# Kernel optimization log

Hardware: AMD Instinct MI355X
Metric: run time of the kernel (lower is better)

## Reference

```python
import jax, jax.numpy as jnp
import numpy as np

N, E, B = 50000, 400000, 8
ND, ED, H, L = 32, 16, 128, 3

def setup_inputs() -> dict:
    key = jax.random.key(0)
    ks = jax.random.split(key, 32)
    s = 0.05
    inp = {
        'x': jax.random.normal(ks[0], (N, ND), jnp.float32),
        'edge_attr': jax.random.normal(ks[1], (E, ED), jnp.float32),
        'global_feature': jax.random.normal(ks[2], (B, 1), jnp.float32),
        'edge_index': jax.random.randint(ks[3], (2, E), 0, N, jnp.int64),
        'batch': jnp.sort(jax.random.randint(ks[4], (N,), 0, B, jnp.int64)),
        # embeddings
        'Wn': jax.random.normal(ks[5], (ND, H), jnp.float32) * s,
        'bn': jnp.zeros((H,), jnp.float32),
        'We': jax.random.normal(ks[6], (ED, H), jnp.float32) * s,
        'be': jnp.zeros((H,), jnp.float32),
        'Wg': jax.random.normal(ks[7], (1, H), jnp.float32) * s,
        'bg': jnp.zeros((H,), jnp.float32),
        # message-passing layers (stacked over L)
        'mW1': jax.random.normal(ks[8], (L, 3 * H, H), jnp.float32) * s,
        'mb1': jnp.zeros((L, H), jnp.float32),
        'mW2': jax.random.normal(ks[9], (L, H, H), jnp.float32) * s,
        'mb2': jnp.zeros((L, H), jnp.float32),
        'uW1': jax.random.normal(ks[10], (L, 2 * H, H), jnp.float32) * s,
        'ub1': jnp.zeros((L, H), jnp.float32),
        'uW2': jax.random.normal(ks[11], (L, H, H), jnp.float32) * s,
        'ub2': jnp.zeros((L, H), jnp.float32),
        # readout MLP
        'rW1': jax.random.normal(ks[12], (2 * H, H), jnp.float32) * s,
        'rb1': jnp.zeros((H,), jnp.float32),
        'rW2': jax.random.normal(ks[13], (H, H // 2), jnp.float32) * s,
        'rb2': jnp.zeros((H // 2,), jnp.float32),
        'rW3': jax.random.normal(ks[14], (H // 2, 1), jnp.float32) * s,
        'rb3': jnp.zeros((1,), jnp.float32),
    }
    return inp

def reference(x, edge_attr, global_feature, Wn, bn, We, be, Wg, bg,
              mW1, mb1, mW2, mb2, uW1, ub1, uW2, ub2,
              rW1, rb1, rW2, rb2, rW3, rb3, edge_index, batch):
    h = x @ Wn + bn                      # [N,H]
    e = edge_attr @ We + be              # [E,H]
    g = global_feature @ Wg + bg         # [B,H]
    src, dst = edge_index[0], edge_index[1]  # PyG: x_j=source, x_i=target, aggregate at target
    for l in range(L):
        m_in = jnp.concatenate([h[dst], h[src], e], axis=1)            # [E,3H]
        m = jax.nn.relu(m_in @ mW1[l] + mb1[l]) @ mW2[l] + mb2[l]       # [E,H]
        aggr = jax.ops.segment_sum(m, dst, num_segments=N)              # [N,H]
        u_in = jnp.concatenate([h, aggr], axis=1)                       # [N,2H]
        upd = jax.nn.relu(u_in @ uW1[l] + ub1[l]) @ uW2[l] + ub2[l]
        h = h + upd
    counts = jax.ops.segment_sum(jnp.ones((N,), h.dtype), batch, num_segments=B)
    pooled = jax.ops.segment_sum(h, batch, num_segments=B) / jnp.maximum(counts, 1.0)[:, None]
    final = jnp.concatenate([pooled, g], axis=1)                        # [B,2H]
    out = jax.nn.relu(final @ rW1 + rb1)
    out = jax.nn.relu(out @ rW2 + rb2)
    return out @ rW3 + rb3                                              # [B,1]
```

## Files before the change

### kernel.cpp

```cpp
#include <hip/hip_runtime.h>

#define NN 50000
#define NPAD 50048
#define NBLK 391
#define NE 400000
#define NBATCH 8
#define NDIM 32
#define EDIM 16
#define H 128
#define NLAYERS 3
#define CHUNK_ELEMS 4096
#define NODE_CHUNKS 24
#define ZW_CHUNK 8192
#define NSB 196
#define ZEB 128

typedef __attribute__((ext_vector_type(8))) __bf16 bf16x8;
typedef __attribute__((ext_vector_type(16))) float f32x16;
typedef __attribute__((ext_vector_type(8))) short short8;
typedef __attribute__((ext_vector_type(2))) float v2f;

__device__ __forceinline__ void block_sync_lds() {
  asm volatile("s_waitcnt lgkmcnt(0)\ns_barrier" ::: "memory");
}
__device__ __forceinline__ void wait_lds() {
  asm volatile("s_waitcnt lgkmcnt(0)" ::: "memory");
}
__device__ __forceinline__ v2f bf2f(unsigned u) {
  v2f r;
  r.x = __uint_as_float(u << 16);
  r.y = __uint_as_float(u & 0xffff0000u);
  return r;
}

__global__ __launch_bounds__(128) void embed_nodes_kernel(
    const float* __restrict__ x, const float* __restrict__ Wn,
    const float* __restrict__ bn, __bf16* __restrict__ hb) {
  __shared__ float Ws[NDIM * H];
  __shared__ float xs[16 * NDIM];
  int j = threadIdx.x;
  int nbase = blockIdx.x * 16;
  for (int r = 0; r < NDIM; ++r) Ws[r * H + j] = Wn[r * H + j];
#pragma unroll
  for (int t = 0; t < 4; ++t) {
    int f = j + t * 128;
    xs[f] = x[nbase * NDIM + f];
  }
  __syncthreads();
  float b = bn[j];
  for (int nn = 0; nn < 16; ++nn) {
    float acc = b;
#pragma unroll
    for (int k = 0; k < NDIM; ++k)
      acc = fmaf(xs[nn * NDIM + k], Ws[k * H + j], acc);
    hb[(size_t)(nbase + nn) * H + j] = (__bf16)acc;
  }
}

__global__ __launch_bounds__(256) void degree_kernel(const int* __restrict__ ei,
                                                     int* __restrict__ deg) {
  int e = blockIdx.x * 256 + threadIdx.x;
  if (e < NE) atomicAdd(&deg[ei[NE + e]], 1);
}

__global__ __launch_bounds__(256) void scan1_kernel(const int* __restrict__ deg,
                                                    int* __restrict__ bsum) {
  __shared__ int ws[4];
  int i = blockIdx.x * 256 + threadIdx.x;
  int lane = threadIdx.x & 63, wid = threadIdx.x >> 6;
  int v = (i < NN) ? deg[i] : 0;
#pragma unroll
  for (int off = 32; off; off >>= 1) v += __shfl_down(v, off);
  if (lane == 0) ws[wid] = v;
  __syncthreads();
  if (threadIdx.x == 0) bsum[blockIdx.x] = ws[0] + ws[1] + ws[2] + ws[3];
}

__global__ __launch_bounds__(256) void scan2_kernel(const int* __restrict__ bsum,
                                                    int* __restrict__ boff) {
  __shared__ int s[256];
  int t = threadIdx.x;
  int v = (t < NSB) ? bsum[t] : 0;
  s[t] = v;
  __syncthreads();
  for (int off = 1; off < 256; off <<= 1) {
    int u = (t >= off) ? s[t - off] : 0;
    __syncthreads();
    s[t] += u;
    __syncthreads();
  }
  if (t < NSB) boff[t] = s[t] - v;
}

__global__ __launch_bounds__(256) void scan3_kernel(const int* __restrict__ deg,
                                                    const int* __restrict__ boff,
                                                    int* __restrict__ cursor) {
  __shared__ int wsum[4], woff[4];
  int i = blockIdx.x * 256 + threadIdx.x;
  int lane = threadIdx.x & 63, wid = threadIdx.x >> 6;
  int orig = (i < NN) ? deg[i] : 0;
  int v = orig;
#pragma unroll
  for (int off = 1; off < 64; off <<= 1) {
    int u = __shfl_up(v, off);
    if (lane >= off) v += u;
  }
  if (lane == 63) wsum[wid] = v;
  __syncthreads();
  if (threadIdx.x == 0) {
    int r = 0;
#pragma unroll
    for (int w = 0; w < 4; ++w) {
      woff[w] = r;
      r += wsum[w];
    }
  }
  __syncthreads();
  if (i < NN) cursor[i] = (v - orig) + woff[wid] + boff[blockIdx.x];
}

__global__ __launch_bounds__(256) void scatter_kernel(
    const int* __restrict__ ei, int* __restrict__ cursor,
    int* __restrict__ srcSrt, int* __restrict__ eidSrt) {
  int e = blockIdx.x * 256 + threadIdx.x;
  if (e < NE) {
    int d = ei[NE + e];
    int pos = atomicAdd(&cursor[d], 1);
    srcSrt[pos] = ei[e];
    eidSrt[pos] = e;
  }
}

__global__ __launch_bounds__(256) void gather_ea_kernel(
    const float* __restrict__ ea, const int* __restrict__ eidSrt,
    __bf16* __restrict__ eaSrt) {
  int fl = blockIdx.x * 256 + threadIdx.x;
  if (fl < NE) {
    int e = eidSrt[fl];
    const float4* ep = (const float4*)(ea + (size_t)e * EDIM);
    __bf16* op = eaSrt + (size_t)fl * EDIM;
#pragma unroll
    for (int q = 0; q < 4; ++q) {
      float4 v = ep[q];
      op[q * 4 + 0] = (__bf16)v.x;
      op[q * 4 + 1] = (__bf16)v.y;
      op[q * 4 + 2] = (__bf16)v.z;
      op[q * 4 + 3] = (__bf16)v.w;
    }
  }
}

__global__ __launch_bounds__(256) void precomp_zw_kernel(
    const float* __restrict__ mW1, __bf16* __restrict__ ZW) {
  int l = blockIdx.x / 8;
  int c = blockIdx.x % 8;
  int tid = threadIdx.x;
  const float* w1 = mW1 + (size_t)l * 384 * H;
  __bf16* dst = ZW + ((size_t)l * 8 + c) * ZW_CHUNK;
  for (int it = 0; it < 32; ++it) {
    int flat = it * 256 + tid;
    int j = flat & 7;
    int lane = (flat >> 3) & 63;
    int nt = (flat >> 9) & 7;
    int hilo = flat >> 12;
    int k = c * 16 + ((lane >> 5) << 3) + j;
    int n = nt * 32 + (lane & 31);
    float w = (n < 128) ? w1[(size_t)k * H + n]
                        : w1[(size_t)(128 + k) * H + (n - 128)];
    __bf16 hi = (__bf16)w;
    __bf16 lo = (__bf16)(w - (float)hi);
    dst[flat] = hilo ? lo : hi;
  }
}

__global__ __launch_bounds__(128) void precomp_wef_kernel(
    const float* __restrict__ mW1, const float* __restrict__ mb1,
    const float* __restrict__ We, const float* __restrict__ be,
    float* __restrict__ Wef, float* __restrict__ bm) {
  int l = blockIdx.x;
  int n = threadIdx.x;
  const float* w1 = mW1 + (size_t)l * 384 * H;
  float acc[EDIM];
#pragma unroll
  for (int i = 0; i < EDIM; ++i) acc[i] = 0.f;
  float accb = 0.f;
  for (int c = 0; c < H; ++c) {
    float wv = w1[(size_t)(256 + c) * H + n];
    accb = fmaf(be[c], wv, accb);
#pragma unroll
    for (int i = 0; i < EDIM; ++i)
      acc[i] = fmaf(We[i * H + c], wv, acc[i]);
  }
#pragma unroll
  for (int i = 0; i < EDIM; ++i)
    Wef[((size_t)l * EDIM + i) * H + n] = acc[i];
  bm[l * H + n] = mb1[l * H + n] + accb;
}

__global__ __launch_bounds__(256) void precomp_wefs_kernel(
    const float* __restrict__ Wef, __bf16* __restrict__ WefS) {
  int l = blockIdx.x;
  int tid = threadIdx.x;
  int nt = tid >> 6, lane = tid & 63;
  int n = nt * 32 + (lane & 31);
  int half = lane >> 5;
  const float* wl = Wef + (size_t)l * EDIM * H;
  __bf16* dst = WefS + (size_t)l * CHUNK_ELEMS;
#pragma unroll
  for (int j = 0; j < 8; ++j) {
    int k = half * 8 + j;
    float w = wl[(size_t)k * H + n];
    __bf16 hi = (__bf16)w;
    __bf16 lo = (__bf16)(w - (float)hi);
    dst[((0 * 4 + nt) * 64 + lane) * 8 + j] = hi;
    dst[((1 * 4 + nt) * 64 + lane) * 8 + j] = lo;
  }
}

__global__ __launch_bounds__(128) void precomp_wu_kernel(
    const float* __restrict__ uW1, const float* __restrict__ mW2,
    const float* __restrict__ mb2, float* __restrict__ Wu,
    float* __restrict__ va) {
  int l = blockIdx.x / 257;
  int r = blockIdx.x % 257;
  int j = threadIdx.x;
  const float* u1 = uW1 + (size_t)l * 256 * H;
  if (r < 128) {
    Wu[((size_t)l * 256 + r) * H + j] = u1[(size_t)r * H + j];
  } else if (r < 256) {
    int i = r - 128;
    const float* m2 = mW2 + ((size_t)l * H + i) * H;
    float s = 0.f;
    for (int c = 0; c < H; ++c)
      s = fmaf(m2[c], u1[(size_t)(128 + c) * H + j], s);
    Wu[((size_t)l * 256 + r) * H + j] = s;
  } else {
    float s = 0.f;
    for (int c = 0; c < H; ++c)
      s = fmaf(mb2[l * H + c], u1[(size_t)(128 + c) * H + j], s);
    va[l * H + j] = s;
  }
}

__global__ __launch_bounds__(256) void precomp_wns_kernel(
    const float* __restrict__ Wu, const float* __restrict__ uW2,
    __bf16* __restrict__ WnS) {
  int l = blockIdx.x / NODE_CHUNKS;
  int c = blockIdx.x % NODE_CHUNKS;
  int tid = threadIdx.x;
  int nt = tid >> 6, lane = tid & 63;
  int n = nt * 32 + (lane & 31);
  int half = lane >> 5;
  __bf16* dst = WnS + ((size_t)l * NODE_CHUNKS + c) * CHUNK_ELEMS;
#pragma unroll
  for (int j = 0; j < 8; ++j) {
    float w;
    if (c < 16) {
      int k = c * 16 + half * 8 + j;
      w = Wu[((size_t)l * 256 + k) * H + n];
    } else {
      int k = (c - 16) * 16 + half * 8 + j;
      w = uW2[((size_t)l * H + k) * H + n];
    }
    __bf16 hi = (__bf16)w;
    __bf16 lo = (__bf16)(w - (float)hi);
    dst[((0 * 4 + nt) * 64 + lane) * 8 + j] = hi;
    dst[((1 * 4 + nt) * 64 + lane) * 8 + j] = lo;
  }
}

__global__ __launch_bounds__(256) void zdzs_kernel(
    const __bf16* __restrict__ hb, const __bf16* __restrict__ ZW,
    const float* __restrict__ bm, __bf16* __restrict__ z) {
  __shared__ __align__(16) __bf16 Bt[2][ZW_CHUNK];
  int tid = threadIdx.x;
  int wid = tid >> 6, lane = tid & 63, m = lane & 31, half = lane >> 5;
  int nb = blockIdx.x * 128;
  int row = nb + wid * 32 + m;
  const __bf16* aH = hb + (size_t)row * H + half * 8;
  const short8* gW = (const short8*)ZW;
  short8* sB0 = (short8*)&Bt[0][0];
  short8* sB1 = (short8*)&Bt[1][0];
#pragma unroll
  for (int q = 0; q < 4; ++q) sB0[tid + q * 256] = gW[tid + q * 256];
  short8 p0 = gW[1024 + tid], p1 = gW[1024 + tid + 256];
  short8 p2 = gW[1024 + tid + 512], p3 = gW[1024 + tid + 768];
  f32x16 acc[8];
#pragma unroll
  for (int nt = 0; nt < 8; ++nt)
#pragma unroll
    for (int r = 0; r < 16; ++r) acc[nt][r] = 0.f;
  bf16x8 a = *(const bf16x8*)aH;
  block_sync_lds();

  for (int s = 0; s < 8; ++s) {
    int buf = s & 1;
    bf16x8 na = a;
    if (s + 1 < 8) na = *(const bf16x8*)(aH + (s + 1) * 16);
    if (s + 1 < 8) {
      short8* sb = buf ? sB0 : sB1;
      sb[tid] = p0;
      sb[tid + 256] = p1;
      sb[tid + 512] = p2;
      sb[tid + 768] = p3;
      if (s + 2 < 8) {
        p0 = gW[(size_t)(s + 2) * 1024 + tid];
        p1 = gW[(size_t)(s + 2) * 1024 + tid + 256];
        p2 = gW[(size_t)(s + 2) * 1024 + tid + 512];
        p3 = gW[(size_t)(s + 2) * 1024 + tid + 768];
      }
    }
    const __bf16* bb = &Bt[buf][0];
#pragma unroll
    for (int nt = 0; nt < 8; ++nt) {
      bf16x8 bh = *(const bf16x8*)&bb[((0 * 8 + nt) * 64 + lane) * 8];
      bf16x8 bl = *(const bf16x8*)&bb[((1 * 8 + nt) * 64 + lane) * 8];
      acc[nt] = __builtin_amdgcn_mfma_f32_32x32x16_bf16(a, bh, acc[nt], 0, 0, 0);
      acc[nt] = __builtin_amdgcn_mfma_f32_32x32x16_bf16(a, bl, acc[nt], 0, 0, 0);
    }
    a = na;
    if (s + 1 < 8) block_sync_lds();
  }

  float bmv[4];
#pragma unroll
  for (int nt = 0; nt < 4; ++nt) bmv[nt] = bm[nt * 32 + m];
#pragma unroll
  for (int nt = 0; nt < 8; ++nt) {
    float bias = (nt < 4) ? bmv[nt] : 0.f;
#pragma unroll
    for (int r = 0; r < 16; ++r) {
      int rowi = (r & 3) + 8 * (r >> 2) + 4 * half;
      z[(size_t)(nb + wid * 32 + rowi) * 256 + nt * 32 + m] =
          (__bf16)(acc[nt][r] + bias);
    }
  }
}

__global__ __launch_bounds__(256) void ze_kernel(
    const __bf16* __restrict__ eaSrt, const __bf16* __restrict__ WefS,
    __bf16* __restrict__ zePre) {
  __shared__ __align__(16) __bf16 Bf[CHUNK_ELEMS];
  int tid = threadIdx.x;
  ((short8*)Bf)[tid] = ((const short8*)WefS)[tid];
  ((short8*)Bf)[tid + 256] = ((const short8*)WefS)[tid + 256];
  int wid = tid >> 6, lane = tid & 63, m = lane & 31, half = lane >> 5;
  int ebase = blockIdx.x * ZEB + wid * 32;
  bf16x8 a = *(const bf16x8*)(eaSrt + (size_t)(ebase + m) * EDIM + half * 8);
  f32x16 acc[4];
#pragma unroll
  for (int nt = 0; nt < 4; ++nt)
#pragma unroll
    for (int r = 0; r < 16; ++r) acc[nt][r] = 0.f;
  block_sync_lds();
#pragma unroll
  for (int nt = 0; nt < 4; ++nt) {
    bf16x8 bh = *(const bf16x8*)&Bf[((0 * 4 + nt) * 64 + lane) * 8];
    bf16x8 bl = *(const bf16x8*)&Bf[((1 * 4 + nt) * 64 + lane) * 8];
    acc[nt] = __builtin_amdgcn_mfma_f32_32x32x16_bf16(a, bh, acc[nt], 0, 0, 0);
    acc[nt] = __builtin_amdgcn_mfma_f32_32x32x16_bf16(a, bl, acc[nt], 0, 0, 0);
  }
#pragma unroll
  for (int nt = 0; nt < 4; ++nt) {
#pragma unroll
    for (int r = 0; r < 16; ++r) {
      int rowi = (r & 3) + 8 * (r >> 2) + 4 * half;
      zePre[(size_t)(ebase + rowi) * H + nt * 32 + m] = (__bf16)acc[nt][r];
    }
  }
}

__global__ __launch_bounds__(256) void edge_aggr_kernel(
    const __bf16* __restrict__ z, const int* __restrict__ srcSrt,
    const int* __restrict__ cend, const __bf16* __restrict__ zePre,
    float* __restrict__ aggrH) {
  int node = blockIdx.x * 4 + (threadIdx.x >> 6);
  int lane = threadIdx.x & 63;
  int c0 = lane * 2;
  int end = cend[node];
  int start = node ? cend[node - 1] : 0;
  v2f acc = {0.f, 0.f};
  if (start < end) {
    v2f zd = bf2f(*(const unsigned*)(z + (size_t)node * 256 + c0));
    int sArr[4];
#pragma unroll
    for (int p = 0; p < 4; ++p)
      if (start + p < end) sArr[p] = srcSrt[start + p];
    for (int e0 = start; e0 < end; e0 += 4) {
      unsigned zsb[4], zeb[4];
#pragma unroll
      for (int p = 0; p < 4; ++p) {
        if (e0 + p < end) {
          zsb[p] = *(const unsigned*)(z + (size_t)sArr[p] * 256 + 128 + c0);
          zeb[p] = *(const unsigned*)(zePre + (size_t)(e0 + p) * H + c0);
        }
      }
#pragma unroll
      for (int p = 0; p < 4; ++p)
        if (e0 + 4 + p < end) sArr[p] = srcSrt[e0 + 4 + p];
#pragma unroll
      for (int p = 0; p < 4; ++p) {
        if (e0 + p < end) {
          v2f t = zd + bf2f(zsb[p]) + bf2f(zeb[p]);
          acc.x += fmaxf(t.x, 0.f);
          acc.y += fmaxf(t.y, 0.f);
        }
      }
    }
  }
  *(v2f*)(aggrH + (size_t)node * H + c0) = acc;
}

__global__ __launch_bounds__(256) void node_update_mfma_kernel(
    __bf16* __restrict__ hb, const float* __restrict__ aggrH,
    const int* __restrict__ deg, const __bf16* __restrict__ WnS,
    const float* __restrict__ ub1, const float* __restrict__ va,
    const float* __restrict__ ub2) {
  __shared__ __align__(16) __bf16 Bt[2][CHUNK_ELEMS];
  __shared__ __bf16 hid[2][32][132];
  __shared__ float degS[64];
  int tid = threadIdx.x;
  int nb = blockIdx.x * 64;
  if (tid < 64) degS[tid] = (float)deg[nb + tid];
  int wid = tid >> 6, lane = tid & 63, m = lane & 31, half = lane >> 5;
  int rg = wid & 1;
  int nh = wid >> 1;
  int row = nb + rg * 32 + m;
  const __bf16* aHb = hb + (size_t)row * H + half * 8;
  const float* aG = aggrH + (size_t)row * H + half * 8;
  const short8* gW = (const short8*)WnS;
  short8* sB0 = (short8*)&Bt[0][0];
  short8* sB1 = (short8*)&Bt[1][0];
  sB0[tid] = gW[tid];
  sB0[tid + 256] = gW[tid + 256];
  short8 p0 = gW[512 + tid], p1 = gW[512 + tid + 256];
  float bv1[2], bva[2];
#pragma unroll
  for (int ntl = 0; ntl < 2; ++ntl) {
    int nt = nh * 2 + ntl;
    bv1[ntl] = ub1[nt * 32 + m];
    bva[ntl] = va[nt * 32 + m];
  }
  f32x16 acc[2];
#pragma unroll
  for (int ntl = 0; ntl < 2; ++ntl)
#pragma unroll
    for (int r = 0; r < 16; ++r) acc[ntl][r] = 0.f;
  bf16x8 acur = *(const bf16x8*)aHb;
  block_sync_lds();

  for (int s = 0; s < 16; ++s) {
    int buf = s & 1;
    bf16x8 anext = acur;
    if (s + 1 < 16) {
      int sp = s + 1;
      if (sp < 8) {
        anext = *(const bf16x8*)(aHb + sp * 16);
      } else {
        const float* pp = aG + (sp - 8) * 16;
        float4 f0 = *(const float4*)pp;
        float4 f1 = *(const float4*)(pp + 4);
        float af[8] = {f0.x, f0.y, f0.z, f0.w, f1.x, f1.y, f1.z, f1.w};
#pragma unroll
        for (int j = 0; j < 8; ++j) anext[j] = (__bf16)af[j];
      }
    }
    {
      short8* sb = buf ? sB0 : sB1;
      sb[tid] = p0;
      sb[tid + 256] = p1;
      if (s + 2 < NODE_CHUNKS) {
        p0 = gW[(size_t)(s + 2) * 512 + tid];
        p1 = gW[(size_t)(s + 2) * 512 + tid + 256];
      }
    }
    const __bf16* bb = &Bt[buf][0];
#pragma unroll
    for (int ntl = 0; ntl < 2; ++ntl) {
      int nt = nh * 2 + ntl;
      bf16x8 bh = *(const bf16x8*)&bb[((0 * 4 + nt) * 64 + lane) * 8];
      bf16x8 bl = *(const bf16x8*)&bb[((1 * 4 + nt) * 64 + lane) * 8];
      acc[ntl] = __builtin_amdgcn_mfma_f32_32x32x16_bf16(acur, bh, acc[ntl], 0, 0, 0);
      acc[ntl] = __builtin_amdgcn_mfma_f32_32x32x16_bf16(acur, bl, acc[ntl], 0, 0, 0);
    }
    acur = anext;
    block_sync_lds();
  }

#pragma unroll
  for (int ntl = 0; ntl < 2; ++ntl) {
    int nt = nh * 2 + ntl;
#pragma unroll
    for (int r = 0; r < 16; ++r) {
      int rowi = (r & 3) + 8 * (r >> 2) + 4 * half;
      float v = acc[ntl][r] + bv1[ntl] + degS[rg * 32 + rowi] * bva[ntl];
      hid[rg][rowi][nt * 32 + m] = (__bf16)fmaxf(v, 0.f);
      acc[ntl][r] = 0.f;
    }
  }
  block_sync_lds();

  for (int s = 16; s < NODE_CHUNKS; ++s) {
    int buf = s & 1;
    if (s + 1 < NODE_CHUNKS) {
      short8* sb = buf ? sB0 : sB1;
      sb[tid] = p0;
      sb[tid + 256] = p1;
      if (s + 2 < NODE_CHUNKS) {
        p0 = gW[(size_t)(s + 2) * 512 + tid];
        p1 = gW[(size_t)(s + 2) * 512 + tid + 256];
      }
    }
    bf16x8 ah = *(const bf16x8*)&hid[rg][m][(s - 16) * 16 + half * 8];
    const __bf16* bb = &Bt[buf][0];
#pragma unroll
    for (int ntl = 0; ntl < 2; ++ntl) {
      int nt = nh * 2 + ntl;
      bf16x8 bh = *(const bf16x8*)&bb[((0 * 4 + nt) * 64 + lane) * 8];
      bf16x8 bl = *(const bf16x8*)&bb[((1 * 4 + nt) * 64 + lane) * 8];
      acc[ntl] = __builtin_amdgcn_mfma_f32_32x32x16_bf16(ah, bh, acc[ntl], 0, 0, 0);
      acc[ntl] = __builtin_amdgcn_mfma_f32_32x32x16_bf16(ah, bl, acc[ntl], 0, 0, 0);
    }
    if (s + 1 < NODE_CHUNKS) block_sync_lds();
  }

#pragma unroll
  for (int ntl = 0; ntl < 2; ++ntl) {
    int nt = nh * 2 + ntl;
    float b2 = ub2[nt * 32 + m];
#pragma unroll
    for (int r = 0; r < 16; ++r) {
      int rowi = (r & 3) + 8 * (r >> 2) + 4 * half;
      size_t idx = (size_t)(nb + rg * 32 + rowi) * H + nt * 32 + m;
      float hv = (float)hb[idx];
      hb[idx] = (__bf16)(hv + acc[ntl][r] + b2);
    }
  }
}

__global__ __launch_bounds__(256) void pool_kernel(
    const __bf16* __restrict__ hb, const int* __restrict__ batch,
    float* __restrict__ pooled, int* __restrict__ counts) {
  __shared__ float pS[NBATCH * H];
  __shared__ int cS[NBATCH];
  int tid = threadIdx.x;
  for (int i = tid; i < NBATCH * H; i += 256) pS[i] = 0.f;
  if (tid < NBATCH) cS[tid] = 0;
  __syncthreads();
  int c = tid & 15;
  int r0 = tid >> 4;
  int nbase = blockIdx.x * 128;
  v2f acc4[4] = {{0.f, 0.f}, {0.f, 0.f}, {0.f, 0.f}, {0.f, 0.f}};
  int cnt = 0;
  int cur = -1;
#pragma unroll
  for (int i = 0; i < 8; ++i) {
    int n = nbase + i * 16 + r0;
    if (n >= NN) break;
    int b = batch[n];
    if (b != cur) {
      if (cur >= 0) {
#pragma unroll
        for (int q = 0; q < 4; ++q) {
          atomicAdd(&pS[cur * H + c * 8 + q * 2], acc4[q].x);
          atomicAdd(&pS[cur * H + c * 8 + q * 2 + 1], acc4[q].y);
          acc4[q].x = 0.f;
          acc4[q].y = 0.f;
        }
        if (c == 0) atomicAdd(&cS[cur], cnt);
        cnt = 0;
      }
      cur = b;
    }
    uint4 v = *(const uint4*)(hb + (size_t)n * H + c * 8);
    acc4[0] += bf2f(v.x);
    acc4[1] += bf2f(v.y);
    acc4[2] += bf2f(v.z);
    acc4[3] += bf2f(v.w);
    cnt++;
  }
  if (cur >= 0) {
#pragma unroll
    for (int q = 0; q < 4; ++q) {
      atomicAdd(&pS[cur * H + c * 8 + q * 2], acc4[q].x);
      atomicAdd(&pS[cur * H + c * 8 + q * 2 + 1], acc4[q].y);
    }
    if (c == 0) atomicAdd(&cS[cur], cnt);
  }
  __syncthreads();
  for (int i = tid; i < NBATCH * H; i += 256) {
    float v = pS[i];
    if (v != 0.f) unsafeAtomicAdd(&pooled[i], v);
  }
  if (tid < NBATCH) {
    int cv = cS[tid];
    if (cv) atomicAdd(&counts[tid], cv);
  }
}

__global__ __launch_bounds__(128) void readout_kernel(
    const float* __restrict__ pooled, const int* __restrict__ counts,
    const float* __restrict__ gf, const float* __restrict__ Wg,
    const float* __restrict__ bg, const float* __restrict__ rW1,
    const float* __restrict__ rb1, const float* __restrict__ rW2,
    const float* __restrict__ rb2, const float* __restrict__ rW3,
    const float* __restrict__ rb3, float* __restrict__ out) {
  __shared__ float fin[256];
  __shared__ float t1[128];
  __shared__ float t2[64];
  int j = threadIdx.x;
  int b = blockIdx.x;
  float cnt = (float)counts[b];
  if (cnt < 1.f) cnt = 1.f;
  fin[j] = pooled[b * H + j] / cnt;
  fin[H + j] = fmaf(gf[b], Wg[j], bg[j]);
  __syncthreads();
  float a = rb1[j];
  for (int k = 0; k < 256; ++k) a = fmaf(fin[k], rW1[k * H + j], a);
  t1[j] = fmaxf(a, 0.f);
  __syncthreads();
  if (j < 64) {
    float a2 = rb2[j];
    for (int k = 0; k < 128; ++k) a2 = fmaf(t1[k], rW2[k * 64 + j], a2);
    t2[j] = fmaxf(a2, 0.f);
  }
  __syncthreads();
  if (j < 64) {
    float p = t2[j] * rW3[j];
#pragma unroll
    for (int off = 32; off; off >>= 1) p += __shfl_down(p, off);
    if (j == 0) out[b] = p + rb3[0];
  }
}

extern "C" void kernel_launch(void* const* d_in, const int* in_sizes, int n_in,
                              void* d_out, int out_size, void* d_ws, size_t ws_size,
                              hipStream_t stream) {
  const float* x   = (const float*)d_in[0];
  const float* ea  = (const float*)d_in[1];
  const float* gf  = (const float*)d_in[2];
  const int*   ei  = (const int*)d_in[3];
  const int*   bat = (const int*)d_in[4];
  const float* Wn  = (const float*)d_in[5];
  const float* bn  = (const float*)d_in[6];
  const float* We  = (const float*)d_in[7];
  const float* be  = (const float*)d_in[8];
  const float* Wg  = (const float*)d_in[9];
  const float* bg  = (const float*)d_in[10];
  const float* mW1 = (const float*)d_in[11];
  const float* mb1 = (const float*)d_in[12];
  const float* mW2 = (const float*)d_in[13];
  const float* mb2 = (const float*)d_in[14];
  const float* uW1 = (const float*)d_in[15];
  const float* ub1 = (const float*)d_in[16];
  const float* uW2 = (const float*)d_in[17];
  const float* ub2 = (const float*)d_in[18];
  const float* rW1 = (const float*)d_in[19];
  const float* rb1 = (const float*)d_in[20];
  const float* rW2 = (const float*)d_in[21];
  const float* rb2 = (const float*)d_in[22];
  const float* rW3 = (const float*)d_in[23];
  const float* rb3 = (const float*)d_in[24];

  char* p = (char*)d_ws;
  __bf16* hb     = (__bf16*)p; p += (size_t)NPAD * H * 2;
  float*  aggrH  = (float*)p;  p += (size_t)NPAD * H * 4;
  __bf16* z      = (__bf16*)p; p += (size_t)NPAD * 256 * 2;
  __bf16* zePre  = (__bf16*)p; p += (size_t)NE * H * 2;
  __bf16* eaSrt  = (__bf16*)p; p += (size_t)NE * EDIM * 2;
  int*    srcSrt = (int*)p;    p += (size_t)NE * 4;
  int*    eidSrt = (int*)p;    p += (size_t)NE * 4;
  __bf16* ZW     = (__bf16*)p; p += (size_t)NLAYERS * 8 * ZW_CHUNK * 2;
  __bf16* WnS    = (__bf16*)p; p += (size_t)NLAYERS * NODE_CHUNKS * CHUNK_ELEMS * 2;
  __bf16* WefS   = (__bf16*)p; p += (size_t)NLAYERS * CHUNK_ELEMS * 2;
  float*  Wef    = (float*)p;  p += (size_t)NLAYERS * EDIM * H * 4;
  float*  bm     = (float*)p;  p += (size_t)NLAYERS * H * 4;
  float*  Wu     = (float*)p;  p += (size_t)NLAYERS * 256 * H * 4;
  float*  va     = (float*)p;  p += (size_t)NLAYERS * H * 4;
  int*    deg    = (int*)p;    p += (size_t)NPAD * 4;
  int*    cursor = (int*)p;    p += (size_t)NPAD * 4;
  int*    bsum   = (int*)p;    p += 256 * 4;
  int*    boff   = (int*)p;    p += 256 * 4;
  float*  pooled = (float*)p;  p += (size_t)NBATCH * H * 4;
  int*    counts = (int*)p;    p += 64;

  hipMemsetAsync(deg, 0, (size_t)NPAD * 4, stream);
  hipMemsetAsync(cursor, 0, (size_t)NPAD * 4, stream);
  hipMemsetAsync(pooled, 0, (size_t)NBATCH * H * 4, stream);
  hipMemsetAsync(counts, 0, 64, stream);

  embed_nodes_kernel<<<NN / 16, 128, 0, stream>>>(x, Wn, bn, hb);
  degree_kernel<<<(NE + 255) / 256, 256, 0, stream>>>(ei, deg);
  scan1_kernel<<<NSB, 256, 0, stream>>>(deg, bsum);
  scan2_kernel<<<1, 256, 0, stream>>>(bsum, boff);
  scan3_kernel<<<NSB, 256, 0, stream>>>(deg, boff, cursor);
  scatter_kernel<<<(NE + 255) / 256, 256, 0, stream>>>(ei, cursor, srcSrt, eidSrt);
  gather_ea_kernel<<<(NE + 255) / 256, 256, 0, stream>>>(ea, eidSrt, eaSrt);
  precomp_zw_kernel<<<NLAYERS * 8, 256, 0, stream>>>(mW1, ZW);
  precomp_wef_kernel<<<NLAYERS, 128, 0, stream>>>(mW1, mb1, We, be, Wef, bm);
  precomp_wefs_kernel<<<NLAYERS, 256, 0, stream>>>(Wef, WefS);
  precomp_wu_kernel<<<NLAYERS * 257, 128, 0, stream>>>(uW1, mW2, mb2, Wu, va);
  precomp_wns_kernel<<<NLAYERS * NODE_CHUNKS, 256, 0, stream>>>(Wu, uW2, WnS);

  for (int l = 0; l < NLAYERS; ++l) {
    zdzs_kernel<<<NBLK, 256, 0, stream>>>(
        hb, ZW + (size_t)l * 8 * ZW_CHUNK, bm + (size_t)l * H, z);
    ze_kernel<<<NE / ZEB, 256, 0, stream>>>(
        eaSrt, WefS + (size_t)l * CHUNK_ELEMS, zePre);
    edge_aggr_kernel<<<NPAD / 4, 256, 0, stream>>>(
        z, srcSrt, cursor, zePre, aggrH);
    node_update_mfma_kernel<<<NPAD / 64, 256, 0, stream>>>(
        hb, aggrH, deg, WnS + (size_t)l * NODE_CHUNKS * CHUNK_ELEMS,
        ub1 + (size_t)l * H, va + (size_t)l * H, ub2 + (size_t)l * H);
  }

  pool_kernel<<<NPAD / 128, 256, 0, stream>>>(hb, bat, pooled, counts);
  readout_kernel<<<NBATCH, 128, 0, stream>>>(pooled, counts, gf, Wg, bg, rW1,
                                             rb1, rW2, rb2, rW3, rb3,
                                             (float*)d_out);
}
```

Measured before the change: 563.8 us.

## Store aggregation in bf16, pack src/eid pairs, split zdzs across N halves

The per-node aggregation buffer is now written as bf16 instead of fp32, which halves its write and read traffic and removes the fp32-to-bf16 conversion in node_update. The sorted source and edge-id arrays are merged into one int2 array. zdzs_kernel now gives each block 64 rows and splits the 256 output columns across wave pairs, so there are twice as many blocks and half the accumulators per wave. The cost is extra rounding of the aggregate before the matmul, and the edge-aggregation kernel now reads 8-byte entries where it needs only the source index.

```diff
diff --git a/kernel.cpp b/kernel.cpp
--- a/kernel.cpp
+++ b/kernel.cpp
@@ -23,9 +23,6 @@
 __device__ __forceinline__ void block_sync_lds() {
   asm volatile("s_waitcnt lgkmcnt(0)\ns_barrier" ::: "memory");
 }
-__device__ __forceinline__ void wait_lds() {
-  asm volatile("s_waitcnt lgkmcnt(0)" ::: "memory");
-}
 __device__ __forceinline__ v2f bf2f(unsigned u) {
   v2f r;
   r.x = __uint_as_float(u << 16);
@@ -121,22 +118,21 @@
 
 __global__ __launch_bounds__(256) void scatter_kernel(
     const int* __restrict__ ei, int* __restrict__ cursor,
-    int* __restrict__ srcSrt, int* __restrict__ eidSrt) {
+    int2* __restrict__ seSrt) {
   int e = blockIdx.x * 256 + threadIdx.x;
   if (e < NE) {
     int d = ei[NE + e];
     int pos = atomicAdd(&cursor[d], 1);
-    srcSrt[pos] = ei[e];
-    eidSrt[pos] = e;
+    seSrt[pos] = make_int2(ei[e], e);
   }
 }
 
 __global__ __launch_bounds__(256) void gather_ea_kernel(
-    const float* __restrict__ ea, const int* __restrict__ eidSrt,
+    const float* __restrict__ ea, const int2* __restrict__ seSrt,
     __bf16* __restrict__ eaSrt) {
   int fl = blockIdx.x * 256 + threadIdx.x;
   if (fl < NE) {
-    int e = eidSrt[fl];
+    int e = seSrt[fl].y;
     const float4* ep = (const float4*)(ea + (size_t)e * EDIM);
     __bf16* op = eaSrt + (size_t)fl * EDIM;
 #pragma unroll
@@ -275,8 +271,10 @@
   __shared__ __align__(16) __bf16 Bt[2][ZW_CHUNK];
   int tid = threadIdx.x;
   int wid = tid >> 6, lane = tid & 63, m = lane & 31, half = lane >> 5;
-  int nb = blockIdx.x * 128;
-  int row = nb + wid * 32 + m;
+  int rg = wid & 1;
+  int nh = wid >> 1;
+  int nb = blockIdx.x * 64;
+  int row = nb + rg * 32 + m;
   const __bf16* aH = hb + (size_t)row * H + half * 8;
   const short8* gW = (const short8*)ZW;
   short8* sB0 = (short8*)&Bt[0][0];
@@ -285,11 +283,11 @@
   for (int q = 0; q < 4; ++q) sB0[tid + q * 256] = gW[tid + q * 256];
   short8 p0 = gW[1024 + tid], p1 = gW[1024 + tid + 256];
   short8 p2 = gW[1024 + tid + 512], p3 = gW[1024 + tid + 768];
-  f32x16 acc[8];
-#pragma unroll
-  for (int nt = 0; nt < 8; ++nt)
-#pragma unroll
-    for (int r = 0; r < 16; ++r) acc[nt][r] = 0.f;
+  f32x16 acc[4];
+#pragma unroll
+  for (int ntl = 0; ntl < 4; ++ntl)
+#pragma unroll
+    for (int r = 0; r < 16; ++r) acc[ntl][r] = 0.f;
   bf16x8 a = *(const bf16x8*)aH;
   block_sync_lds();
 
@@ -312,11 +310,12 @@
     }
     const __bf16* bb = &Bt[buf][0];
 #pragma unroll
-    for (int nt = 0; nt < 8; ++nt) {
+    for (int ntl = 0; ntl < 4; ++ntl) {
+      int nt = nh * 4 + ntl;
       bf16x8 bh = *(const bf16x8*)&bb[((0 * 8 + nt) * 64 + lane) * 8];
       bf16x8 bl = *(const bf16x8*)&bb[((1 * 8 + nt) * 64 + lane) * 8];
-      acc[nt] = __builtin_amdgcn_mfma_f32_32x32x16_bf16(a, bh, acc[nt], 0, 0, 0);
-      acc[nt] = __builtin_amdgcn_mfma_f32_32x32x16_bf16(a, bl, acc[nt], 0, 0, 0);
+      acc[ntl] = __builtin_amdgcn_mfma_f32_32x32x16_bf16(a, bh, acc[ntl], 0, 0, 0);
+      acc[ntl] = __builtin_amdgcn_mfma_f32_32x32x16_bf16(a, bl, acc[ntl], 0, 0, 0);
     }
     a = na;
     if (s + 1 < 8) block_sync_lds();
@@ -324,15 +323,18 @@
 
   float bmv[4];
 #pragma unroll
-  for (int nt = 0; nt < 4; ++nt) bmv[nt] = bm[nt * 32 + m];
-#pragma unroll
-  for (int nt = 0; nt < 8; ++nt) {
-    float bias = (nt < 4) ? bmv[nt] : 0.f;
+  for (int ntl = 0; ntl < 4; ++ntl) {
+    int nt = nh * 4 + ntl;
+    bmv[ntl] = (nt < 4) ? bm[nt * 32 + m] : 0.f;
+  }
+#pragma unroll
+  for (int ntl = 0; ntl < 4; ++ntl) {
+    int nt = nh * 4 + ntl;
 #pragma unroll
     for (int r = 0; r < 16; ++r) {
       int rowi = (r & 3) + 8 * (r >> 2) + 4 * half;
-      z[(size_t)(nb + wid * 32 + rowi) * 256 + nt * 32 + m] =
-          (__bf16)(acc[nt][r] + bias);
+      z[(size_t)(nb + rg * 32 + rowi) * 256 + nt * 32 + m] =
+          (__bf16)(acc[ntl][r] + bmv[ntl]);
     }
   }
 }
@@ -371,9 +373,9 @@
 }
 
 __global__ __launch_bounds__(256) void edge_aggr_kernel(
-    const __bf16* __restrict__ z, const int* __restrict__ srcSrt,
+    const __bf16* __restrict__ z, const int2* __restrict__ seSrt,
     const int* __restrict__ cend, const __bf16* __restrict__ zePre,
-    float* __restrict__ aggrH) {
+    __bf16* __restrict__ aggrB) {
   int node = blockIdx.x * 4 + (threadIdx.x >> 6);
   int lane = threadIdx.x & 63;
   int c0 = lane * 2;
@@ -385,7 +387,7 @@
     int sArr[4];
 #pragma unroll
     for (int p = 0; p < 4; ++p)
-      if (start + p < end) sArr[p] = srcSrt[start + p];
+      if (start + p < end) sArr[p] = seSrt[start + p].x;
     for (int e0 = start; e0 < end; e0 += 4) {
       unsigned zsb[4], zeb[4];
 #pragma unroll
@@ -397,7 +399,7 @@
       }
 #pragma unroll
       for (int p = 0; p < 4; ++p)
-        if (e0 + 4 + p < end) sArr[p] = srcSrt[e0 + 4 + p];
+        if (e0 + 4 + p < end) sArr[p] = seSrt[e0 + 4 + p].x;
 #pragma unroll
       for (int p = 0; p < 4; ++p) {
         if (e0 + p < end) {
@@ -408,11 +410,14 @@
       }
     }
   }
-  *(v2f*)(aggrH + (size_t)node * H + c0) = acc;
+  union { __bf16 b[2]; unsigned u; } pk;
+  pk.b[0] = (__bf16)acc.x;
+  pk.b[1] = (__bf16)acc.y;
+  *(unsigned*)(aggrB + (size_t)node * H + c0) = pk.u;
 }
 
 __global__ __launch_bounds__(256) void node_update_mfma_kernel(
-    __bf16* __restrict__ hb, const float* __restrict__ aggrH,
+    __bf16* __restrict__ hb, const __bf16* __restrict__ aggrB,
     const int* __restrict__ deg, const __bf16* __restrict__ WnS,
     const float* __restrict__ ub1, const float* __restrict__ va,
     const float* __restrict__ ub2) {
@@ -427,7 +432,7 @@
   int nh = wid >> 1;
   int row = nb + rg * 32 + m;
   const __bf16* aHb = hb + (size_t)row * H + half * 8;
-  const float* aG = aggrH + (size_t)row * H + half * 8;
+  const __bf16* aGb = aggrB + (size_t)row * H + half * 8;
   const short8* gW = (const short8*)WnS;
   short8* sB0 = (short8*)&Bt[0][0];
   short8* sB1 = (short8*)&Bt[1][0];
@@ -454,16 +459,8 @@
     bf16x8 anext = acur;
     if (s + 1 < 16) {
       int sp = s + 1;
-      if (sp < 8) {
-        anext = *(const bf16x8*)(aHb + sp * 16);
-      } else {
-        const float* pp = aG + (sp - 8) * 16;
-        float4 f0 = *(const float4*)pp;
-        float4 f1 = *(const float4*)(pp + 4);
-        float af[8] = {f0.x, f0.y, f0.z, f0.w, f1.x, f1.y, f1.z, f1.w};
-#pragma unroll
-        for (int j = 0; j < 8; ++j) anext[j] = (__bf16)af[j];
-      }
+      anext = (sp < 8) ? *(const bf16x8*)(aHb + sp * 16)
+                       : *(const bf16x8*)(aGb + (sp - 8) * 16);
     }
     {
       short8* sb = buf ? sB0 : sB1;
@@ -664,12 +661,11 @@
 
   char* p = (char*)d_ws;
   __bf16* hb     = (__bf16*)p; p += (size_t)NPAD * H * 2;
-  float*  aggrH  = (float*)p;  p += (size_t)NPAD * H * 4;
+  __bf16* aggrB  = (__bf16*)p; p += (size_t)NPAD * H * 2;
   __bf16* z      = (__bf16*)p; p += (size_t)NPAD * 256 * 2;
   __bf16* zePre  = (__bf16*)p; p += (size_t)NE * H * 2;
   __bf16* eaSrt  = (__bf16*)p; p += (size_t)NE * EDIM * 2;
-  int*    srcSrt = (int*)p;    p += (size_t)NE * 4;
-  int*    eidSrt = (int*)p;    p += (size_t)NE * 4;
+  int2*   seSrt  = (int2*)p;   p += (size_t)NE * 8;
   __bf16* ZW     = (__bf16*)p; p += (size_t)NLAYERS * 8 * ZW_CHUNK * 2;
   __bf16* WnS    = (__bf16*)p; p += (size_t)NLAYERS * NODE_CHUNKS * CHUNK_ELEMS * 2;
   __bf16* WefS   = (__bf16*)p; p += (size_t)NLAYERS * CHUNK_ELEMS * 2;
@@ -694,8 +690,8 @@
   scan1_kernel<<<NSB, 256, 0, stream>>>(deg, bsum);
   scan2_kernel<<<1, 256, 0, stream>>>(bsum, boff);
   scan3_kernel<<<NSB, 256, 0, stream>>>(deg, boff, cursor);
-  scatter_kernel<<<(NE + 255) / 256, 256, 0, stream>>>(ei, cursor, srcSrt, eidSrt);
-  gather_ea_kernel<<<(NE + 255) / 256, 256, 0, stream>>>(ea, eidSrt, eaSrt);
+  scatter_kernel<<<(NE + 255) / 256, 256, 0, stream>>>(ei, cursor, seSrt);
+  gather_ea_kernel<<<(NE + 255) / 256, 256, 0, stream>>>(ea, seSrt, eaSrt);
   precomp_zw_kernel<<<NLAYERS * 8, 256, 0, stream>>>(mW1, ZW);
   precomp_wef_kernel<<<NLAYERS, 128, 0, stream>>>(mW1, mb1, We, be, Wef, bm);
   precomp_wefs_kernel<<<NLAYERS, 256, 0, stream>>>(Wef, WefS);
@@ -703,14 +699,14 @@
   precomp_wns_kernel<<<NLAYERS * NODE_CHUNKS, 256, 0, stream>>>(Wu, uW2, WnS);
 
   for (int l = 0; l < NLAYERS; ++l) {
-    zdzs_kernel<<<NBLK, 256, 0, stream>>>(
+    zdzs_kernel<<<NPAD / 64, 256, 0, stream>>>(
         hb, ZW + (size_t)l * 8 * ZW_CHUNK, bm + (size_t)l * H, z);
     ze_kernel<<<NE / ZEB, 256, 0, stream>>>(
         eaSrt, WefS + (size_t)l * CHUNK_ELEMS, zePre);
     edge_aggr_kernel<<<NPAD / 4, 256, 0, stream>>>(
-        z, srcSrt, cursor, zePre, aggrH);
+        z, seSrt, cursor, zePre, aggrB);
     node_update_mfma_kernel<<<NPAD / 64, 256, 0, stream>>>(
-        hb, aggrH, deg, WnS + (size_t)l * NODE_CHUNKS * CHUNK_ELEMS,
+        hb, aggrB, deg, WnS + (size_t)l * NODE_CHUNKS * CHUNK_ELEMS,
         ub1 + (size_t)l * H, va + (size_t)l * H, ub2 + (size_t)l * H);
   }
 
```

New measurement: 546.3 us. -3.1%, faster.
